# Kernel tuning notes

Measured on AMD Instinct MI355X. Metric: run time of the kernel, lower is better.

Reference implementation:

```python
import jax, jax.numpy as jnp
import numpy as np

P = 16           # patch size
E = P * P        # embed dim of MHA (must equal dim)
NH = 4           # num heads
HD = E // NH     # head dim


def setup_inputs() -> dict:
    key = jax.random.key(0)
    k1, k2, k3, k4, k5 = jax.random.split(key, 5)
    B, C, H, W = 2, 256, 256, 256
    scale = 1.0 / np.sqrt(E)
    return {
        "x": jax.random.normal(k1, (B, C, H, W), dtype=jnp.float32),
        "w_in": jax.random.normal(k2, (3 * E, E), dtype=jnp.float32) * scale,
        "b_in": jnp.zeros((3 * E,), dtype=jnp.float32),
        "w_out": jax.random.normal(k3, (E, E), dtype=jnp.float32) * scale,
        "b_out": jnp.zeros((E,), dtype=jnp.float32),
    }


def reference(x, w_in, b_in, w_out, b_out):
    B, C, H, W = x.shape
    nP = (H // P) * (W // P)
    # x.unfold(2,p,p).unfold(3,p,p).reshape(B,C,-1,p*p)
    patches = (
        x.reshape(B, C, H // P, P, W // P, P)
        .transpose(0, 1, 2, 4, 3, 5)
        .reshape(B, C, nP, E)
    )
    # permute(0,2,1,3).reshape(B*nP, C, p*p): batch=B*nP, seq=C, embed=E
    t = patches.transpose(0, 2, 1, 3).reshape(B * nP, C, E)

    qkv = t @ w_in.T + b_in                      # (N, C, 3E)
    q, k, v = jnp.split(qkv, 3, axis=-1)

    def to_heads(a):  # (N, C, E) -> (N, NH, C, HD)
        return a.reshape(B * nP, C, NH, HD).transpose(0, 2, 1, 3)

    q, k, v = to_heads(q), to_heads(k), to_heads(v)
    scores = jnp.einsum("nhqd,nhkd->nhqk", q * (HD ** -0.5), k)
    attn = jax.nn.softmax(scores, axis=-1)
    o = jnp.einsum("nhqk,nhkd->nhqd", attn, v)   # (N, NH, C, HD)
    o = o.transpose(0, 2, 1, 3).reshape(B * nP, C, E)
    o = o @ w_out.T + b_out
    # reshape(B, -1, C, p*p).permute(0, 2, 1, 3)
    return o.reshape(B, nP, C, E).transpose(0, 2, 1, 3)
```

## Files before the change

### kernel.cpp

```cpp
#include <hip/hip_runtime.h>
#include <hip/hip_bf16.h>

typedef __attribute__((ext_vector_type(8))) short s16x8;
typedef __attribute__((ext_vector_type(4))) float f32x4;

#define WS_SEG 67108864ULL

#if defined(__has_attribute)
#if __has_attribute(amdgpu_num_vgpr)
#define VGPR_CAP_128 __attribute__((amdgpu_num_vgpr(128)))
#else
#define VGPR_CAP_128
#endif
#else
#define VGPR_CAP_128
#endif

static __device__ __forceinline__ unsigned short f2bf(float f) {
    return __builtin_bit_cast(unsigned short, __float2bfloat16(f));
}
static __device__ __forceinline__ unsigned int pack2(float a, float b) {
    return (unsigned int)f2bf(a) | ((unsigned int)f2bf(b) << 16);
}
static __device__ __forceinline__ s16x8 u4cast(uint4 u) {
    return __builtin_bit_cast(s16x8, u);
}
static __device__ __forceinline__ void gl_lds16(const void* g, void* l) {
    __builtin_amdgcn_global_load_lds(
        (const __attribute__((address_space(1))) unsigned int*)g,
        (__attribute__((address_space(3))) unsigned int*)l, 16, 0, 0);
}

__global__ __launch_bounds__(256) void convw_swz(const float* __restrict__ wi,
                                                 unsigned short* __restrict__ wb) {
    int i = (blockIdx.x * 256 + threadIdx.x) * 4;
    float4 v = *reinterpret_cast<const float4*>(wi + i);
    int bb = i * 2;
    int row = i >> 8;
    int dst = (bb & ~127) | ((bb & 127) ^ ((row & 7) << 4));
    uint2 o = { pack2(v.x, v.y), pack2(v.z, v.w) };
    *reinterpret_cast<uint2*>((char*)wb + dst) = o;
}

__global__ __launch_bounds__(256) void gather_swz(const float* __restrict__ x,
                                                  unsigned short* __restrict__ t) {
    int q = (blockIdx.x * 256 + threadIdx.x) * 4;
    int e = q & 255, c = (q >> 8) & 255, n = q >> 16;
    int b = n >> 8, p = n & 255;
    int xi = ((b * 256 + c) * 256 + (p >> 4) * 16 + (e >> 4)) * 256 + (p & 15) * 16 + (e & 15);
    float4 v = *reinterpret_cast<const float4*>(x + xi);
    int bb = q * 2;
    int row = q >> 8;
    int dst = (bb & ~127) | ((bb & 127) ^ ((row & 7) << 4));
    uint2 o = { pack2(v.x, v.y), pack2(v.z, v.w) };
    *reinterpret_cast<uint2*>((char*)t + dst) = o;
}

template<int MODE>
__global__ __launch_bounds__(256) void gemm6(
    const unsigned short* __restrict__ Ab,
    const unsigned short* __restrict__ Wb,
    const float* __restrict__ bias,
    unsigned short* __restrict__ Qo, unsigned short* __restrict__ Ko,
    unsigned short* __restrict__ Vt, float* __restrict__ Out)
{
    __shared__ __align__(16) char smem[32768];
    char* AsB = smem;
    char* BsB = smem + 16384;

    const int t = threadIdx.x, w = t >> 6, lane = t & 63;
    const int lr = lane & 15, lk = lane >> 4;
    const int wm = w >> 1, wn = w & 1;

    constexpr int NB = (MODE == 0) ? 4 : 2;
    const int flat = blockIdx.x;
    const int xcd = flat & 7, idx = flat >> 3;
    const int bm = xcd * 128 + idx / NB;
    const int bn = idx % NB;

    const char* Ag = (const char*)Ab + (size_t)bm * 65536;
    const char* Bg = (const char*)Wb + (size_t)bn * 65536;

    f32x4 acc[4][4] = {};

    for (int kk = 0; kk < 4; ++kk) {
        #pragma unroll
        for (int i = 0; i < 4; ++i) {
            int u = (i * 4 + w) * 64 + lane;
            int row = u >> 3, cb = (u & 7) * 16;
            gl_lds16(Ag + row * 512 + kk * 128 + cb, AsB + (i * 4 + w) * 1024);
            gl_lds16(Bg + row * 512 + kk * 128 + cb, BsB + (i * 4 + w) * 1024);
        }
        __syncthreads();
        #pragma unroll
        for (int kc = 0; kc < 2; ++kc) {
            s16x8 af[4], bf[4];
            #pragma unroll
            for (int fm = 0; fm < 4; ++fm) {
                int r = wm * 64 + fm * 16 + lr;
                af[fm] = *reinterpret_cast<const s16x8*>(
                    AsB + r * 128 + ((kc * 64 + lk * 16) ^ ((r & 7) << 4)));
            }
            #pragma unroll
            for (int fn = 0; fn < 4; ++fn) {
                int cc = wn * 64 + fn * 16 + lr;
                bf[fn] = *reinterpret_cast<const s16x8*>(
                    BsB + cc * 128 + ((kc * 64 + lk * 16) ^ ((cc & 7) << 4)));
            }
            #pragma unroll
            for (int fm = 0; fm < 4; ++fm)
                #pragma unroll
                for (int fn = 0; fn < 4; ++fn) {
                    if (MODE == 1)
                        acc[fm][fn] = __builtin_amdgcn_mfma_f32_16x16x32_bf16(af[fm], bf[fn], acc[fm][fn], 0, 0, 0);
                    else
                        acc[fm][fn] = __builtin_amdgcn_mfma_f32_16x16x32_bf16(bf[fn], af[fm], acc[fm][fn], 0, 0, 0);
                }
        }
        if (kk < 3) __syncthreads();
    }

    const int n = bm >> 1;

    if (MODE == 0) {
        unsigned short* base = (bn >> 1) ? Ko : Qo;
        const int h0 = (bn & 1) * 2;
        const float qs = (bn >> 1) ? 1.0f : 0.18033688011112042f;
        #pragma unroll
        for (int fn = 0; fn < 4; ++fn) {
            int col_local = wn * 64 + fn * 16 + lk * 4;
            f32x4 bv4 = *reinterpret_cast<const f32x4*>(bias + bn * 128 + col_local);
            int h = h0 + (col_local >> 6), d0 = col_local & 63;
            #pragma unroll
            for (int fm = 0; fm < 4; ++fm) {
                int c = (bm & 1) * 128 + wm * 64 + fm * 16 + lr;
                uint2 st = { pack2((acc[fm][fn][0] + bv4[0]) * qs, (acc[fm][fn][1] + bv4[1]) * qs),
                             pack2((acc[fm][fn][2] + bv4[2]) * qs, (acc[fm][fn][3] + bv4[3]) * qs) };
                *reinterpret_cast<uint2*>(
                    (char*)base + (size_t)((n * 4 + h) * 256 + c) * 128 + d0 * 2) = st;
            }
        }
    } else if (MODE == 1) {
        const int h0 = bn * 2;
        #pragma unroll
        for (int fn = 0; fn < 4; ++fn) {
            int col_local = wn * 64 + fn * 16 + lr;
            float bv = bias[bn * 128 + col_local];
            int hl = col_local >> 6, d = col_local & 63;
            #pragma unroll
            for (int fm = 0; fm < 4; ++fm) {
                int c = (bm & 1) * 128 + wm * 64 + fm * 16 + lk * 4;
                uint2 st = { pack2(acc[fm][fn][0] + bv, acc[fm][fn][1] + bv),
                             pack2(acc[fm][fn][2] + bv, acc[fm][fn][3] + bv) };
                *reinterpret_cast<uint2*>(
                    (char*)Vt + (size_t)((n * 4 + h0 + hl) * 64 + d) * 512 + c * 2) = st;
            }
        }
    } else {
        #pragma unroll
        for (int fn = 0; fn < 4; ++fn) {
            int colg = bn * 128 + wn * 64 + fn * 16 + lk * 4;
            f32x4 bv4 = *reinterpret_cast<const f32x4*>(bias + colg);
            #pragma unroll
            for (int fm = 0; fm < 4; ++fm) {
                int rg = bm * 128 + wm * 64 + fm * 16 + lr;
                int nn = rg >> 8, c = rg & 255;
                int b = nn >> 8, p = nn & 255;
                f32x4 st = acc[fm][fn] + bv4;
                *reinterpret_cast<f32x4*>(
                    Out + (((size_t)(b * 256 + c) * 256 + p) << 8) + colg) = st;
            }
        }
    }
}

__global__ __launch_bounds__(1024) VGPR_CAP_128 void attn8(
    const unsigned short* __restrict__ Q,
    const unsigned short* __restrict__ K,
    const unsigned short* __restrict__ V,
    unsigned short* __restrict__ O)
{
    __shared__ __align__(16) char KsB[32768];
    __shared__ __align__(16) char VsB[32768];

    const int nh = blockIdx.x;
    const int n = nh >> 2, h = nh & 3;
    const int t = threadIdx.x, w = t >> 6, lane = t & 63;
    const int lr = lane & 15, lk = lane >> 4;

    const unsigned short* Qg = Q + (size_t)nh * 16384;
    const char* Kg = (const char*)K + (size_t)nh * 32768;
    const char* Vg = (const char*)V + (size_t)nh * 32768;

    #pragma unroll
    for (int i = 0; i < 2; ++i) {
        int u = i * 1024 + t;
        int row = u >> 3, cb = (u & 7) * 16;
        uint4 val = *reinterpret_cast<const uint4*>(Kg + u * 16);
        *reinterpret_cast<uint4*>(KsB + row * 128 + (cb ^ ((row & 7) << 4))) = val;
    }
    #pragma unroll
    for (int i = 0; i < 2; ++i) {
        int u = i * 1024 + t;
        int row = u >> 5, cb = (u & 31) * 16;
        uint4 val = *reinterpret_cast<const uint4*>(Vg + u * 16);
        *reinterpret_cast<uint4*>(VsB + row * 512 + (cb ^ ((row & 7) << 4))) = val;
    }
    __syncthreads();

    const int swz = (lr & 7) << 4;
    const int qt = w;

    s16x8 bq0 = *reinterpret_cast<const s16x8*>(Qg + (qt * 16 + lr) * 64 + lk * 8);
    s16x8 bq1 = *reinterpret_cast<const s16x8*>(Qg + (qt * 16 + lr) * 64 + 32 + lk * 8);

    f32x4 oacc[4] = {};
    float l = 0.f;

    #pragma unroll
    for (int kb = 0; kb < 8; ++kb) {
        const int rb0 = ((2 * kb) * 16 + lr) * 128;
        const int rb1 = ((2 * kb + 1) * 16 + lr) * 128;
        s16x8 a00 = *reinterpret_cast<const s16x8*>(KsB + rb0 + ((lk * 16) ^ swz));
        s16x8 a01 = *reinterpret_cast<const s16x8*>(KsB + rb0 + ((64 + lk * 16) ^ swz));
        s16x8 a10 = *reinterpret_cast<const s16x8*>(KsB + rb1 + ((lk * 16) ^ swz));
        s16x8 a11 = *reinterpret_cast<const s16x8*>(KsB + rb1 + ((64 + lk * 16) ^ swz));
        f32x4 s0 = { 0.f, 0.f, 0.f, 0.f }, s1 = { 0.f, 0.f, 0.f, 0.f };
        __builtin_amdgcn_s_setprio(1);
        s0 = __builtin_amdgcn_mfma_f32_16x16x32_bf16(a00, bq0, s0, 0, 0, 0);
        s0 = __builtin_amdgcn_mfma_f32_16x16x32_bf16(a01, bq1, s0, 0, 0, 0);
        s1 = __builtin_amdgcn_mfma_f32_16x16x32_bf16(a10, bq0, s1, 0, 0, 0);
        s1 = __builtin_amdgcn_mfma_f32_16x16x32_bf16(a11, bq1, s1, 0, 0, 0);
        __builtin_amdgcn_s_setprio(0);

        float p0 = exp2f(s0[0]), p1 = exp2f(s0[1]);
        float p2 = exp2f(s0[2]), p3 = exp2f(s0[3]);
        float p4 = exp2f(s1[0]), p5 = exp2f(s1[1]);
        float p6 = exp2f(s1[2]), p7 = exp2f(s1[3]);
        l += ((p0 + p1) + (p2 + p3)) + ((p4 + p5) + (p6 + p7));
        uint4 pk = { pack2(p0, p1), pack2(p2, p3), pack2(p4, p5), pack2(p6, p7) };
        s16x8 pf = u4cast(pk);

        __builtin_amdgcn_s_setprio(1);
        #pragma unroll
        for (int dt = 0; dt < 4; ++dt) {
            const char* vb = VsB + (dt * 16 + lr) * 512;
            uint2 v0 = *reinterpret_cast<const uint2*>(vb + ((kb * 64 + lk * 8) ^ swz));
            uint2 v1 = *reinterpret_cast<const uint2*>(vb + ((kb * 64 + lk * 8 + 32) ^ swz));
            uint4 uu = { v0.x, v0.y, v1.x, v1.y };
            oacc[dt] = __builtin_amdgcn_mfma_f32_16x16x32_bf16(u4cast(uu), pf, oacc[dt], 0, 0, 0);
        }
        __builtin_amdgcn_s_setprio(0);
    }

    l += __shfl_xor(l, 16);
    l += __shfl_xor(l, 32);
    const float rl = 1.0f / l;

    char* orow = (char*)O + (size_t)(n * 256 + qt * 16 + lr) * 512 + h * 128;
    #pragma unroll
    for (int dt = 0; dt < 4; ++dt) {
        uint2 st = { pack2(oacc[dt][0] * rl, oacc[dt][1] * rl),
                     pack2(oacc[dt][2] * rl, oacc[dt][3] * rl) };
        *reinterpret_cast<uint2*>(orow + ((dt * 32 + lk * 8) ^ swz)) = st;
    }
}

extern "C" void kernel_launch(void* const* d_in, const int* in_sizes, int n_in,
                              void* d_out, int out_size, void* d_ws, size_t ws_size,
                              hipStream_t stream) {
    const float* x     = (const float*)d_in[0];
    const float* w_in  = (const float*)d_in[1];
    const float* b_in  = (const float*)d_in[2];
    const float* w_out = (const float*)d_in[3];
    const float* b_out = (const float*)d_in[4];

    char* ws = (char*)d_ws;
    unsigned short* tO = (unsigned short*)(ws);
    unsigned short* Qw = (unsigned short*)(ws + WS_SEG);
    unsigned short* Kw = (unsigned short*)(ws + 2 * WS_SEG);
    unsigned short* Vw = (unsigned short*)(ws + 3 * WS_SEG);

    unsigned short* WbIn = (unsigned short*)((float*)d_out + out_size - 98304);

    convw_swz<<<192, 256, 0, stream>>>(w_in, WbIn);
    gather_swz<<<32768, 256, 0, stream>>>(x, tO);

    gemm6<0><<<4096, 256, 0, stream>>>(tO, WbIn, b_in, Qw, Kw, nullptr, nullptr);
    gemm6<1><<<2048, 256, 0, stream>>>(tO, WbIn + 512 * 256, b_in + 512,
                                       nullptr, nullptr, Vw, nullptr);

    attn8<<<2048, 1024, 0, stream>>>(Qw, Kw, Vw, tO);

    unsigned short* WbOut = Kw;
    convw_swz<<<64, 256, 0, stream>>>(w_out, WbOut);

    gemm6<2><<<2048, 256, 0, stream>>>(tO, WbOut, b_out,
                                       nullptr, nullptr, nullptr, (float*)d_out);
}
```

Measured before the change: 283.3 us.

## Double-buffer GEMM LDS tiles and fuse QKV projections into one launch

```diff
diff --git a/kernel.cpp b/kernel.cpp
--- a/kernel.cpp
+++ b/kernel.cpp
@@ -57,22 +57,22 @@
 }
 
 template<int MODE>
-__global__ __launch_bounds__(256) void gemm6(
+__global__ __launch_bounds__(256) void gemm8(
     const unsigned short* __restrict__ Ab,
     const unsigned short* __restrict__ Wb,
     const float* __restrict__ bias,
     unsigned short* __restrict__ Qo, unsigned short* __restrict__ Ko,
     unsigned short* __restrict__ Vt, float* __restrict__ Out)
 {
-    __shared__ __align__(16) char smem[32768];
+    __shared__ __align__(16) char smem[65536];
     char* AsB = smem;
-    char* BsB = smem + 16384;
+    char* BsB = smem + 32768;
 
     const int t = threadIdx.x, w = t >> 6, lane = t & 63;
     const int lr = lane & 15, lk = lane >> 4;
     const int wm = w >> 1, wn = w & 1;
 
-    constexpr int NB = (MODE == 0) ? 4 : 2;
+    constexpr int NB = (MODE == 0) ? 6 : 2;
     const int flat = blockIdx.x;
     const int xcd = flat & 7, idx = flat >> 3;
     const int bm = xcd * 128 + idx / NB;
@@ -81,17 +81,28 @@
     const char* Ag = (const char*)Ab + (size_t)bm * 65536;
     const char* Bg = (const char*)Wb + (size_t)bn * 65536;
 
-    f32x4 acc[4][4] = {};
-
-    for (int kk = 0; kk < 4; ++kk) {
+    const bool swapped = (MODE == 1) || (bn < 4);
+
+    auto stage = [&](int kk) {
+        char* Ad = AsB + (kk & 1) * 16384;
+        char* Bd = BsB + (kk & 1) * 16384;
         #pragma unroll
         for (int i = 0; i < 4; ++i) {
             int u = (i * 4 + w) * 64 + lane;
             int row = u >> 3, cb = (u & 7) * 16;
-            gl_lds16(Ag + row * 512 + kk * 128 + cb, AsB + (i * 4 + w) * 1024);
-            gl_lds16(Bg + row * 512 + kk * 128 + cb, BsB + (i * 4 + w) * 1024);
-        }
+            gl_lds16(Ag + row * 512 + kk * 128 + cb, Ad + (i * 4 + w) * 1024);
+            gl_lds16(Bg + row * 512 + kk * 128 + cb, Bd + (i * 4 + w) * 1024);
+        }
+    };
+
+    f32x4 acc[4][4] = {};
+
+    stage(0);
+    for (int kk = 0; kk < 4; ++kk) {
         __syncthreads();
+        if (kk < 3) stage(kk + 1);
+        const char* Ac = AsB + (kk & 1) * 16384;
+        const char* Bc = BsB + (kk & 1) * 16384;
         #pragma unroll
         for (int kc = 0; kc < 2; ++kc) {
             s16x8 af[4], bf[4];
@@ -99,61 +110,66 @@
             for (int fm = 0; fm < 4; ++fm) {
                 int r = wm * 64 + fm * 16 + lr;
                 af[fm] = *reinterpret_cast<const s16x8*>(
-                    AsB + r * 128 + ((kc * 64 + lk * 16) ^ ((r & 7) << 4)));
+                    Ac + r * 128 + ((kc * 64 + lk * 16) ^ ((r & 7) << 4)));
             }
             #pragma unroll
             for (int fn = 0; fn < 4; ++fn) {
                 int cc = wn * 64 + fn * 16 + lr;
                 bf[fn] = *reinterpret_cast<const s16x8*>(
-                    BsB + cc * 128 + ((kc * 64 + lk * 16) ^ ((cc & 7) << 4)));
-            }
-            #pragma unroll
-            for (int fm = 0; fm < 4; ++fm)
+                    Bc + cc * 128 + ((kc * 64 + lk * 16) ^ ((cc & 7) << 4)));
+            }
+            if (swapped) {
                 #pragma unroll
-                for (int fn = 0; fn < 4; ++fn) {
-                    if (MODE == 1)
+                for (int fm = 0; fm < 4; ++fm)
+                    #pragma unroll
+                    for (int fn = 0; fn < 4; ++fn)
+                        acc[fm][fn] = __builtin_amdgcn_mfma_f32_16x16x32_bf16(bf[fn], af[fm], acc[fm][fn], 0, 0, 0);
+            } else {
+                #pragma unroll
+                for (int fm = 0; fm < 4; ++fm)
+                    #pragma unroll
+                    for (int fn = 0; fn < 4; ++fn)
                         acc[fm][fn] = __builtin_amdgcn_mfma_f32_16x16x32_bf16(af[fm], bf[fn], acc[fm][fn], 0, 0, 0);
-                    else
-                        acc[fm][fn] = __builtin_amdgcn_mfma_f32_16x16x32_bf16(bf[fn], af[fm], acc[fm][fn], 0, 0, 0);
+            }
+        }
+    }
+
+    const int n = bm >> 1;
+
+    if (MODE == 0) {
+        if (bn < 4) {
+            unsigned short* base = (bn >> 1) ? Ko : Qo;
+            const int h0 = (bn & 1) * 2;
+            const float qs = (bn >> 1) ? 1.0f : 0.18033688011112042f;
+            #pragma unroll
+            for (int fn = 0; fn < 4; ++fn) {
+                int col_local = wn * 64 + fn * 16 + lk * 4;
+                f32x4 bv4 = *reinterpret_cast<const f32x4*>(bias + bn * 128 + col_local);
+                int h = h0 + (col_local >> 6), d0 = col_local & 63;
+                #pragma unroll
+                for (int fm = 0; fm < 4; ++fm) {
+                    int c = (bm & 1) * 128 + wm * 64 + fm * 16 + lr;
+                    uint2 st = { pack2((acc[fm][fn][0] + bv4[0]) * qs, (acc[fm][fn][1] + bv4[1]) * qs),
+                                 pack2((acc[fm][fn][2] + bv4[2]) * qs, (acc[fm][fn][3] + bv4[3]) * qs) };
+                    *reinterpret_cast<uint2*>(
+                        (char*)base + (size_t)((n * 4 + h) * 256 + c) * 128 + d0 * 2) = st;
                 }
-        }
-        if (kk < 3) __syncthreads();
-    }
-
-    const int n = bm >> 1;
-
-    if (MODE == 0) {
-        unsigned short* base = (bn >> 1) ? Ko : Qo;
-        const int h0 = (bn & 1) * 2;
-        const float qs = (bn >> 1) ? 1.0f : 0.18033688011112042f;
-        #pragma unroll
-        for (int fn = 0; fn < 4; ++fn) {
-            int col_local = wn * 64 + fn * 16 + lk * 4;
-            f32x4 bv4 = *reinterpret_cast<const f32x4*>(bias + bn * 128 + col_local);
-            int h = h0 + (col_local >> 6), d0 = col_local & 63;
-            #pragma unroll
-            for (int fm = 0; fm < 4; ++fm) {
-                int c = (bm & 1) * 128 + wm * 64 + fm * 16 + lr;
-                uint2 st = { pack2((acc[fm][fn][0] + bv4[0]) * qs, (acc[fm][fn][1] + bv4[1]) * qs),
-                             pack2((acc[fm][fn][2] + bv4[2]) * qs, (acc[fm][fn][3] + bv4[3]) * qs) };
-                *reinterpret_cast<uint2*>(
-                    (char*)base + (size_t)((n * 4 + h) * 256 + c) * 128 + d0 * 2) = st;
-            }
-        }
-    } else if (MODE == 1) {
-        const int h0 = bn * 2;
-        #pragma unroll
-        for (int fn = 0; fn < 4; ++fn) {
-            int col_local = wn * 64 + fn * 16 + lr;
-            float bv = bias[bn * 128 + col_local];
-            int hl = col_local >> 6, d = col_local & 63;
-            #pragma unroll
-            for (int fm = 0; fm < 4; ++fm) {
-                int c = (bm & 1) * 128 + wm * 64 + fm * 16 + lk * 4;
-                uint2 st = { pack2(acc[fm][fn][0] + bv, acc[fm][fn][1] + bv),
-                             pack2(acc[fm][fn][2] + bv, acc[fm][fn][3] + bv) };
-                *reinterpret_cast<uint2*>(
-                    (char*)Vt + (size_t)((n * 4 + h0 + hl) * 64 + d) * 512 + c * 2) = st;
+            }
+        } else {
+            const int h0 = (bn - 4) * 2;
+            #pragma unroll
+            for (int fn = 0; fn < 4; ++fn) {
+                int col_local = wn * 64 + fn * 16 + lr;
+                float bv = bias[bn * 128 + col_local];
+                int hl = col_local >> 6, d = col_local & 63;
+                #pragma unroll
+                for (int fm = 0; fm < 4; ++fm) {
+                    int c = (bm & 1) * 128 + wm * 64 + fm * 16 + lk * 4;
+                    uint2 st = { pack2(acc[fm][fn][0] + bv, acc[fm][fn][1] + bv),
+                                 pack2(acc[fm][fn][2] + bv, acc[fm][fn][3] + bv) };
+                    *reinterpret_cast<uint2*>(
+                        (char*)Vt + (size_t)((n * 4 + h0 + hl) * 64 + d) * 512 + c * 2) = st;
+                }
             }
         }
     } else {
@@ -286,15 +302,13 @@
     convw_swz<<<192, 256, 0, stream>>>(w_in, WbIn);
     gather_swz<<<32768, 256, 0, stream>>>(x, tO);
 
-    gemm6<0><<<4096, 256, 0, stream>>>(tO, WbIn, b_in, Qw, Kw, nullptr, nullptr);
-    gemm6<1><<<2048, 256, 0, stream>>>(tO, WbIn + 512 * 256, b_in + 512,
-                                       nullptr, nullptr, Vw, nullptr);
+    gemm8<0><<<6144, 256, 0, stream>>>(tO, WbIn, b_in, Qw, Kw, Vw, nullptr);
 
     attn8<<<2048, 1024, 0, stream>>>(Qw, Kw, Vw, tO);
 
     unsigned short* WbOut = Kw;
     convw_swz<<<64, 256, 0, stream>>>(w_out, WbOut);
 
-    gemm6<2><<<2048, 256, 0, stream>>>(tO, WbOut, b_out,
+    gemm8<1><<<2048, 256, 0, stream>>>(tO, WbOut, b_out,
                                        nullptr, nullptr, nullptr, (float*)d_out);
 }
```

After: 289.2 us. 1.02x slower.

## Fuse QKV projection into one kernel keeping activation tile resident in LDS

Applied to the files above, without the earlier changes.

```diff
diff --git a/kernel.cpp b/kernel.cpp
--- a/kernel.cpp
+++ b/kernel.cpp
@@ -29,6 +29,21 @@
     __builtin_amdgcn_global_load_lds(
         (const __attribute__((address_space(1))) unsigned int*)g,
         (__attribute__((address_space(3))) unsigned int*)l, 16, 0, 0);
+}
+
+__global__ __launch_bounds__(256) void convw_frag(const float* __restrict__ wi,
+                                                  unsigned short* __restrict__ wp) {
+    int o8 = blockIdx.x * 256 + threadIdx.x;
+    int nkc = o8 >> 10;
+    int rem = o8 & 1023;
+    int row = rem >> 2;
+    int lk8 = (rem & 3) * 8;
+    int Ni = nkc >> 3, kk = (nkc >> 1) & 3, kc = nkc & 1;
+    const float* src = wi + ((size_t)(Ni * 256 + row)) * 256 + kk * 64 + kc * 32 + lk8;
+    float4 a = *reinterpret_cast<const float4*>(src);
+    float4 b = *reinterpret_cast<const float4*>(src + 4);
+    uint4 o = { pack2(a.x, a.y), pack2(a.z, a.w), pack2(b.x, b.y), pack2(b.z, b.w) };
+    *reinterpret_cast<uint4*>(wp + o8 * 8) = o;
 }
 
 __global__ __launch_bounds__(256) void convw_swz(const float* __restrict__ wi,
@@ -56,81 +71,70 @@
     *reinterpret_cast<uint2*>((char*)t + dst) = o;
 }
 
-template<int MODE>
-__global__ __launch_bounds__(256) void gemm6(
+__global__ __launch_bounds__(256) void qkv11(
     const unsigned short* __restrict__ Ab,
-    const unsigned short* __restrict__ Wb,
+    const unsigned short* __restrict__ Wp,
     const float* __restrict__ bias,
     unsigned short* __restrict__ Qo, unsigned short* __restrict__ Ko,
-    unsigned short* __restrict__ Vt, float* __restrict__ Out)
+    unsigned short* __restrict__ Vt)
 {
-    __shared__ __align__(16) char smem[32768];
-    char* AsB = smem;
-    char* BsB = smem + 16384;
+    __shared__ __align__(16) char AsB[65536];
 
     const int t = threadIdx.x, w = t >> 6, lane = t & 63;
     const int lr = lane & 15, lk = lane >> 4;
     const int wm = w >> 1, wn = w & 1;
 
-    constexpr int NB = (MODE == 0) ? 4 : 2;
-    const int flat = blockIdx.x;
-    const int xcd = flat & 7, idx = flat >> 3;
-    const int bm = xcd * 128 + idx / NB;
-    const int bn = idx % NB;
+    const int bm = blockIdx.x;
+    const int n = bm >> 1;
 
     const char* Ag = (const char*)Ab + (size_t)bm * 65536;
-    const char* Bg = (const char*)Wb + (size_t)bn * 65536;
-
-    f32x4 acc[4][4] = {};
-
-    for (int kk = 0; kk < 4; ++kk) {
-        #pragma unroll
-        for (int i = 0; i < 4; ++i) {
-            int u = (i * 4 + w) * 64 + lane;
-            int row = u >> 3, cb = (u & 7) * 16;
-            gl_lds16(Ag + row * 512 + kk * 128 + cb, AsB + (i * 4 + w) * 1024);
-            gl_lds16(Bg + row * 512 + kk * 128 + cb, BsB + (i * 4 + w) * 1024);
-        }
-        __syncthreads();
-        #pragma unroll
-        for (int kc = 0; kc < 2; ++kc) {
-            s16x8 af[4], bf[4];
-            #pragma unroll
-            for (int fm = 0; fm < 4; ++fm) {
-                int r = wm * 64 + fm * 16 + lr;
-                af[fm] = *reinterpret_cast<const s16x8*>(
-                    AsB + r * 128 + ((kc * 64 + lk * 16) ^ ((r & 7) << 4)));
-            }
-            #pragma unroll
-            for (int fn = 0; fn < 4; ++fn) {
-                int cc = wn * 64 + fn * 16 + lr;
-                bf[fn] = *reinterpret_cast<const s16x8*>(
-                    BsB + cc * 128 + ((kc * 64 + lk * 16) ^ ((cc & 7) << 4)));
-            }
-            #pragma unroll
-            for (int fm = 0; fm < 4; ++fm)
-                #pragma unroll
-                for (int fn = 0; fn < 4; ++fn) {
-                    if (MODE == 1)
-                        acc[fm][fn] = __builtin_amdgcn_mfma_f32_16x16x32_bf16(af[fm], bf[fn], acc[fm][fn], 0, 0, 0);
-                    else
-                        acc[fm][fn] = __builtin_amdgcn_mfma_f32_16x16x32_bf16(bf[fn], af[fm], acc[fm][fn], 0, 0, 0);
+
+    #pragma unroll
+    for (int i = 0; i < 16; ++i) {
+        int u = i * 256 + t;
+        gl_lds16(Ag + u * 16, AsB + (i * 256 + w * 64) * 16);
+    }
+    __syncthreads();
+
+    #pragma unroll 1
+    for (int bn = 0; bn < 4; ++bn) {
+        const int X = bn >> 1;
+        const int half = bn & 1;
+        f32x4 acc[4][4] = {};
+        #pragma unroll
+        for (int kk = 0; kk < 4; ++kk) {
+            #pragma unroll
+            for (int kc = 0; kc < 2; ++kc) {
+                const char* wb = (const char*)Wp + (((X * 4 + kk) * 2 + kc) << 14);
+                s16x8 bfr[4];
+                #pragma unroll
+                for (int fn = 0; fn < 4; ++fn)
+                    bfr[fn] = *reinterpret_cast<const s16x8*>(
+                        wb + ((half * 128 + wn * 64 + fn * 16 + lr) * 32 + lk * 8) * 2);
+                s16x8 af[4];
+                #pragma unroll
+                for (int fm = 0; fm < 4; ++fm) {
+                    int m = wm * 64 + fm * 16 + lr;
+                    af[fm] = *reinterpret_cast<const s16x8*>(
+                        AsB + m * 512 + kk * 128 + ((kc * 64 + lk * 16) ^ ((m & 7) << 4)));
                 }
-        }
-        if (kk < 3) __syncthreads();
-    }
-
-    const int n = bm >> 1;
-
-    if (MODE == 0) {
-        unsigned short* base = (bn >> 1) ? Ko : Qo;
-        const int h0 = (bn & 1) * 2;
-        const float qs = (bn >> 1) ? 1.0f : 0.18033688011112042f;
+                __builtin_amdgcn_s_setprio(1);
+                #pragma unroll
+                for (int fm = 0; fm < 4; ++fm)
+                    #pragma unroll
+                    for (int fn = 0; fn < 4; ++fn)
+                        acc[fm][fn] = __builtin_amdgcn_mfma_f32_16x16x32_bf16(bfr[fn], af[fm], acc[fm][fn], 0, 0, 0);
+                __builtin_amdgcn_s_setprio(0);
+            }
+        }
+        unsigned short* base = X ? Ko : Qo;
+        const float qs = X ? 1.0f : 0.18033688011112042f;
         #pragma unroll
         for (int fn = 0; fn < 4; ++fn) {
             int col_local = wn * 64 + fn * 16 + lk * 4;
-            f32x4 bv4 = *reinterpret_cast<const f32x4*>(bias + bn * 128 + col_local);
-            int h = h0 + (col_local >> 6), d0 = col_local & 63;
+            int mc = half * 128 + col_local;
+            f32x4 bv4 = *reinterpret_cast<const f32x4*>(bias + X * 256 + mc);
+            int h = mc >> 6, d0 = mc & 63;
             #pragma unroll
             for (int fm = 0; fm < 4; ++fm) {
                 int c = (bm & 1) * 128 + wm * 64 + fm * 16 + lr;
@@ -140,36 +144,124 @@
                     (char*)base + (size_t)((n * 4 + h) * 256 + c) * 128 + d0 * 2) = st;
             }
         }
-    } else if (MODE == 1) {
-        const int h0 = bn * 2;
+    }
+
+    #pragma unroll 1
+    for (int half = 0; half < 2; ++half) {
+        f32x4 acc[4][4] = {};
+        #pragma unroll
+        for (int kk = 0; kk < 4; ++kk) {
+            #pragma unroll
+            for (int kc = 0; kc < 2; ++kc) {
+                const char* wb = (const char*)Wp + (((2 * 4 + kk) * 2 + kc) << 14);
+                s16x8 bfr[4];
+                #pragma unroll
+                for (int fn = 0; fn < 4; ++fn)
+                    bfr[fn] = *reinterpret_cast<const s16x8*>(
+                        wb + ((half * 128 + wn * 64 + fn * 16 + lr) * 32 + lk * 8) * 2);
+                s16x8 af[4];
+                #pragma unroll
+                for (int fm = 0; fm < 4; ++fm) {
+                    int m = wm * 64 + fm * 16 + lr;
+                    af[fm] = *reinterpret_cast<const s16x8*>(
+                        AsB + m * 512 + kk * 128 + ((kc * 64 + lk * 16) ^ ((m & 7) << 4)));
+                }
+                __builtin_amdgcn_s_setprio(1);
+                #pragma unroll
+                for (int fm = 0; fm < 4; ++fm)
+                    #pragma unroll
+                    for (int fn = 0; fn < 4; ++fn)
+                        acc[fm][fn] = __builtin_amdgcn_mfma_f32_16x16x32_bf16(af[fm], bfr[fn], acc[fm][fn], 0, 0, 0);
+                __builtin_amdgcn_s_setprio(0);
+            }
+        }
         #pragma unroll
         for (int fn = 0; fn < 4; ++fn) {
-            int col_local = wn * 64 + fn * 16 + lr;
-            float bv = bias[bn * 128 + col_local];
-            int hl = col_local >> 6, d = col_local & 63;
+            int dcol_local = wn * 64 + fn * 16 + lr;
+            int mc = half * 128 + dcol_local;
+            float bv = bias[512 + mc];
+            int h = mc >> 6, d = mc & 63;
             #pragma unroll
             for (int fm = 0; fm < 4; ++fm) {
                 int c = (bm & 1) * 128 + wm * 64 + fm * 16 + lk * 4;
                 uint2 st = { pack2(acc[fm][fn][0] + bv, acc[fm][fn][1] + bv),
                              pack2(acc[fm][fn][2] + bv, acc[fm][fn][3] + bv) };
                 *reinterpret_cast<uint2*>(
-                    (char*)Vt + (size_t)((n * 4 + h0 + hl) * 64 + d) * 512 + c * 2) = st;
-            }
-        }
-    } else {
-        #pragma unroll
-        for (int fn = 0; fn < 4; ++fn) {
-            int colg = bn * 128 + wn * 64 + fn * 16 + lk * 4;
-            f32x4 bv4 = *reinterpret_cast<const f32x4*>(bias + colg);
+                    (char*)Vt + (size_t)((n * 4 + h) * 64 + d) * 512 + c * 2) = st;
+            }
+        }
+    }
+}
+
+__global__ __launch_bounds__(256) void gemm_out(
+    const unsigned short* __restrict__ Ab,
+    const unsigned short* __restrict__ Wb,
+    const float* __restrict__ bias,
+    float* __restrict__ Out)
+{
+    __shared__ __align__(16) char smem[32768];
+    char* AsB = smem;
+    char* BsB = smem + 16384;
+
+    const int t = threadIdx.x, w = t >> 6, lane = t & 63;
+    const int lr = lane & 15, lk = lane >> 4;
+    const int wm = w >> 1, wn = w & 1;
+
+    const int flat = blockIdx.x;
+    const int xcd = flat & 7, idx = flat >> 3;
+    const int bm = xcd * 128 + idx / 2;
+    const int bn = idx % 2;
+
+    const char* Ag = (const char*)Ab + (size_t)bm * 65536;
+    const char* Bg = (const char*)Wb + (size_t)bn * 65536;
+
+    f32x4 acc[4][4] = {};
+
+    for (int kk = 0; kk < 4; ++kk) {
+        #pragma unroll
+        for (int i = 0; i < 4; ++i) {
+            int u = (i * 4 + w) * 64 + lane;
+            int row = u >> 3, cb = (u & 7) * 16;
+            gl_lds16(Ag + row * 512 + kk * 128 + cb, AsB + (i * 4 + w) * 1024);
+            gl_lds16(Bg + row * 512 + kk * 128 + cb, BsB + (i * 4 + w) * 1024);
+        }
+        __syncthreads();
+        #pragma unroll
+        for (int kc = 0; kc < 2; ++kc) {
+            s16x8 af[4], bf[4];
             #pragma unroll
             for (int fm = 0; fm < 4; ++fm) {
-                int rg = bm * 128 + wm * 64 + fm * 16 + lr;
-                int nn = rg >> 8, c = rg & 255;
-                int b = nn >> 8, p = nn & 255;
-                f32x4 st = acc[fm][fn] + bv4;
-                *reinterpret_cast<f32x4*>(
-                    Out + (((size_t)(b * 256 + c) * 256 + p) << 8) + colg) = st;
-            }
+                int r = wm * 64 + fm * 16 + lr;
+                af[fm] = *reinterpret_cast<const s16x8*>(
+                    AsB + r * 128 + ((kc * 64 + lk * 16) ^ ((r & 7) << 4)));
+            }
+            #pragma unroll
+            for (int fn = 0; fn < 4; ++fn) {
+                int cc = wn * 64 + fn * 16 + lr;
+                bf[fn] = *reinterpret_cast<const s16x8*>(
+                    BsB + cc * 128 + ((kc * 64 + lk * 16) ^ ((cc & 7) << 4)));
+            }
+            #pragma unroll
+            for (int fm = 0; fm < 4; ++fm)
+                #pragma unroll
+                for (int fn = 0; fn < 4; ++fn)
+                    acc[fm][fn] = __builtin_amdgcn_mfma_f32_16x16x32_bf16(bf[fn], af[fm], acc[fm][fn], 0, 0, 0);
+        }
+        if (kk < 3) __syncthreads();
+    }
+
+    #pragma unroll
+    for (int fn = 0; fn < 4; ++fn) {
+        int colg = bn * 128 + wn * 64 + fn * 16 + lk * 4;
+        f32x4 bv4 = *reinterpret_cast<const f32x4*>(bias + colg);
+        #pragma unroll
+        for (int fm = 0; fm < 4; ++fm) {
+            int rg = bm * 128 + wm * 64 + fm * 16 + lr;
+            int nn = rg >> 8, c = rg & 255;
+            int b = nn >> 8, p = nn & 255;
+            f32x4 st = acc[fm][fn] + bv4;
+            *reinterpret_cast<f32x4*>(
+                Out + (((size_t)(b * 256 + c) * 256 + p) << 8) + colg) = st;
         }
     }
 }
@@ -283,18 +375,15 @@
 
     unsigned short* WbIn = (unsigned short*)((float*)d_out + out_size - 98304);
 
-    convw_swz<<<192, 256, 0, stream>>>(w_in, WbIn);
+    convw_frag<<<96, 256, 0, stream>>>(w_in, WbIn);
     gather_swz<<<32768, 256, 0, stream>>>(x, tO);
 
-    gemm6<0><<<4096, 256, 0, stream>>>(tO, WbIn, b_in, Qw, Kw, nullptr, nullptr);
-    gemm6<1><<<2048, 256, 0, stream>>>(tO, WbIn + 512 * 256, b_in + 512,
-                                       nullptr, nullptr, Vw, nullptr);
+    qkv11<<<1024, 256, 0, stream>>>(tO, WbIn, b_in, Qw, Kw, Vw);
 
     attn8<<<2048, 1024, 0, stream>>>(Qw, Kw, Vw, tO);
 
     unsigned short* WbOut = Kw;
     convw_swz<<<64, 256, 0, stream>>>(w_out, WbOut);
 
-    gemm6<2><<<2048, 256, 0, stream>>>(tO, WbOut, b_out,
-                                       nullptr, nullptr, nullptr, (float*)d_out);
-}
+    gemm_out<<<2048, 256, 0, stream>>>(tO, WbOut, b_out, (float*)d_out);
+}
```

Result: slower. 321.7 us (+13.6%).
